# Performance work log

Hardware: AMD Instinct MI355X
Metric: run time of the kernel (lower is better)

## Reference

```python
import jax, jax.numpy as jnp
import numpy as np

BETA = 0.8
THRESHOLD = 1.0

@jax.custom_vjp
def surrogate_spike(m):
    return (m >= THRESHOLD).astype(m.dtype)

def _spike_fwd(m):
    return surrogate_spike(m), m

def _spike_bwd(m, g):
    s = jax.nn.sigmoid(4.0 * (m - THRESHOLD))
    return (g * s * (1.0 - s) * 4.0,)

surrogate_spike.defvjp(_spike_fwd, _spike_bwd)

def setup_inputs() -> dict:
    key = jax.random.key(0)
    k1, k2, k3, k4 = jax.random.split(key, 4)
    B, T, D, F = 4, 2048, 1024, 4096
    x = jax.random.normal(k1, (B, T, D), dtype=jnp.float32)
    Wg = jax.random.normal(k2, (F, D), dtype=jnp.float32) * (1.0 / np.sqrt(D))
    Wu = jax.random.normal(k3, (F, D), dtype=jnp.float32) * (1.0 / np.sqrt(D))
    Wd = jax.random.normal(k4, (D, F), dtype=jnp.float32) * (1.0 / np.sqrt(F))
    theta = jnp.ones((F,), dtype=jnp.float32) * THRESHOLD
    return {"x": x, "Wg": Wg, "Wu": Wu, "Wd": Wd, "theta": theta}

def reference(x, Wg, Wu, Wd, theta):
    # x: [B,T,D]; Wg,Wu: [F,D]; Wd: [D,F]; theta: [F]
    gate_input = jnp.einsum('btd,fd->btf', x, Wg)  # [B,T,F]

    def step(membrane, g_t):
        membrane = BETA * membrane + g_t           # leaky integrate
        spike = surrogate_spike(membrane)          # threshold fire
        membrane = membrane - theta * spike        # reset
        return membrane, spike

    B, T, F = gate_input.shape
    V0 = jnp.zeros((B, F), dtype=x.dtype)
    _, spikes = jax.lax.scan(step, V0, jnp.swapaxes(gate_input, 0, 1))  # [T,B,F]
    gate = jnp.swapaxes(spikes, 0, 1)              # [B,T,F]

    up = jnp.einsum('btd,fd->btf', x, Wu)
    return jnp.einsum('btf,df->btd', gate * jax.nn.silu(up), Wd)
```

## Files before the change

kernel.cpp:

```cpp
#include <hip/hip_runtime.h>
#include <hip/hip_bf16.h>
#include <math.h>


namespace {

constexpr int B_ = 4;
constexpr int T_ = 2048;
constexpr int D_ = 1024;
constexpr int F_ = 4096;
constexpr int TC = 512;
constexpr int NCHUNK = T_ / TC;
constexpr int MC = B_ * TC;
constexpr int LDK = 40;

typedef __attribute__((ext_vector_type(8))) short bf16x8;
typedef __attribute__((ext_vector_type(4))) float f32x4;
typedef __attribute__((ext_vector_type(2))) float f32x2;

#define PK_FMA_LO(accv, av, bv)                                         \
  asm("v_pk_fma_f32 %0, %1, %2, %0 op_sel:[0,0,0] op_sel_hi:[1,0,1]"    \
      : "+v"(accv) : "v"(av), "v"(bv))
#define PK_FMA_HI(accv, av, bv)                                         \
  asm("v_pk_fma_f32 %0, %1, %2, %0 op_sel:[0,1,0] op_sel_hi:[1,1,1]"    \
      : "+v"(accv) : "v"(av), "v"(bv))

__device__ __forceinline__ float silu_f(float u) {
  return u / (1.0f + expf(-u));
}

__device__ __forceinline__ int map_row(int r, int t0) {
  return (r >> 9) * T_ + t0 + (r & (TC - 1));
}

__device__ __forceinline__ unsigned short bf16_rn(float x) {
  unsigned int u = __float_as_uint(x);
  u += 0x7FFF + ((u >> 16) & 1);
  return (unsigned short)(u >> 16);
}
__device__ __forceinline__ float bf16_f(unsigned short h) {
  unsigned int u = ((unsigned int)h) << 16;
  return __uint_as_float(u);
}

__device__ __forceinline__ void async_copy16(const float* g, float* l) {
  __builtin_amdgcn_global_load_lds(
      (const __attribute__((address_space(1))) void*)g,
      (__attribute__((address_space(3))) void*)l, 16, 0, 0);
}

__global__ __launch_bounds__(256)
void transpose_wg(const float* __restrict__ Wg, float* __restrict__ WgT) {
  __shared__ float tile[32][33];
  const int tx = threadIdx.x & 31, ty = threadIdx.x >> 5;
  const int d0 = blockIdx.x * 32, f0 = blockIdx.y * 32;
#pragma unroll
  for (int i = 0; i < 4; ++i)
    tile[ty + i * 8][tx] = Wg[(size_t)(f0 + ty + i * 8) * D_ + d0 + tx];
  __syncthreads();
#pragma unroll
  for (int i = 0; i < 4; ++i)
    WgT[(size_t)(d0 + ty + i * 8) * F_ + f0 + tx] = tile[tx][ty + i * 8];
}

__global__ __launch_bounds__(256)
void transpose_x(const float* __restrict__ x, float* __restrict__ xT, int t0) {
  __shared__ float tile[32][33];
  const int tx = threadIdx.x & 31, ty = threadIdx.x >> 5;
  const int d0 = blockIdx.x * 32, r0 = blockIdx.y * 32;
#pragma unroll
  for (int i = 0; i < 4; ++i)
    tile[ty + i * 8][tx] =
        x[(size_t)map_row(r0 + ty + i * 8, t0) * D_ + d0 + tx];
  __syncthreads();
#pragma unroll
  for (int i = 0; i < 4; ++i)
    xT[(size_t)(d0 + ty + i * 8) * MC + r0 + tx] = tile[tx][ty + i * 8];
}

#pragma clang fp contract(off)
__global__ __launch_bounds__(512)
void gemm_gate_np(const float* __restrict__ xT, const float* __restrict__ WgT,
                  float* __restrict__ G) {
  __shared__ float As[32 * 128];
  __shared__ float Bs[32 * 128];
  const int tid = threadIdx.x;
  const int lane = tid & 63;
  const int w = tid >> 6;
  const int tx = tid & 31;
  const int ty = tid >> 5;
  const int row0 = blockIdx.y * 128;
  const int col0 = blockIdx.x * 128;

  f32x2 accP[4][4];
  f32x2 csumP[4][4];
#pragma unroll
  for (int i = 0; i < 4; ++i)
#pragma unroll
    for (int j = 0; j < 4; ++j) {
      accP[i][j] = (f32x2)0.0f;
      csumP[i][j] = (f32x2)0.0f;
    }

  for (int kt = 0; kt < D_; kt += 32) {
    if (kt != 0 && (kt & 127) == 0) {
#pragma unroll
      for (int i = 0; i < 4; ++i)
#pragma unroll
        for (int j = 0; j < 4; ++j) {
          csumP[i][j].x = __fadd_rn(csumP[i][j].x, accP[i][j].x);
          csumP[i][j].y = __fadd_rn(csumP[i][j].y, accP[i][j].y);
          accP[i][j] = (f32x2)0.0f;
        }
    }
    __syncthreads();
#pragma unroll
    for (int t = 0; t < 2; ++t) {
      const int ii = w * 2 + t;
      const int kr = kt + ii * 2 + (lane >> 5);
      async_copy16(&xT[(size_t)kr * MC + row0 + (lane & 31) * 4],
                   &As[ii * 256]);
    }
#pragma unroll
    for (int t = 0; t < 2; ++t) {
      const int ii = w * 2 + t;
      const int kr = kt + ii * 2 + (lane >> 5);
      async_copy16(&WgT[(size_t)kr * F_ + col0 + (lane & 31) * 4],
                   &Bs[ii * 256]);
    }
    __syncthreads();
#pragma unroll
    for (int kk = 0; kk < 32; ++kk) {
      const float4 a0 = *reinterpret_cast<const float4*>(&As[kk * 128 + ty * 8]);
      const float4 a1 = *reinterpret_cast<const float4*>(&As[kk * 128 + ty * 8 + 4]);
      const float4 b0 = *reinterpret_cast<const float4*>(&Bs[kk * 128 + tx * 4]);
      f32x2 ap[4];
      ap[0] = (f32x2){a0.x, a0.y};
      ap[1] = (f32x2){a0.z, a0.w};
      ap[2] = (f32x2){a1.x, a1.y};
      ap[3] = (f32x2){a1.z, a1.w};
      const f32x2 bp0 = (f32x2){b0.x, b0.y};
      const f32x2 bp1 = (f32x2){b0.z, b0.w};
#pragma unroll
      for (int ip = 0; ip < 4; ++ip) {
        PK_FMA_LO(accP[ip][0], ap[ip], bp0);
        PK_FMA_HI(accP[ip][1], ap[ip], bp0);
        PK_FMA_LO(accP[ip][2], ap[ip], bp1);
        PK_FMA_HI(accP[ip][3], ap[ip], bp1);
      }
    }
  }

#pragma unroll
  for (int ip = 0; ip < 4; ++ip) {
#pragma unroll
    for (int h = 0; h < 2; ++h) {
      const int r = row0 + ty * 8 + ip * 2 + h;
      float4 v;
      v.x = __fadd_rn(h ? csumP[ip][0].y : csumP[ip][0].x,
                      h ? accP[ip][0].y : accP[ip][0].x);
      v.y = __fadd_rn(h ? csumP[ip][1].y : csumP[ip][1].x,
                      h ? accP[ip][1].y : accP[ip][1].x);
      v.z = __fadd_rn(h ? csumP[ip][2].y : csumP[ip][2].x,
                      h ? accP[ip][2].y : accP[ip][2].x);
      v.w = __fadd_rn(h ? csumP[ip][3].y : csumP[ip][3].x,
                      h ? accP[ip][3].y : accP[ip][3].x);
      *reinterpret_cast<float4*>(&G[(size_t)r * F_ + col0 + tx * 4]) = v;
    }
  }
}
#pragma clang fp contract(fast)

#pragma clang fp contract(off)
__global__ __launch_bounds__(64)
void lif_scan(const float* __restrict__ G, unsigned char* __restrict__ S8,
              float* __restrict__ state, const float* __restrict__ theta,
              int t0) {
  const int j = blockIdx.x * 64 + threadIdx.x;
  const int f = j & (F_ - 1);
  const int b = j >> 12;
  float m = (t0 == 0) ? 0.0f : state[j];
  const float th = theta[f];
  const size_t base = (size_t)b * TC * F_ + f;
  for (int tb = 0; tb < TC; tb += 16) {
    float g[16];
#pragma unroll
    for (int u = 0; u < 16; ++u) g[u] = G[base + (size_t)(tb + u) * F_];
#pragma unroll
    for (int u = 0; u < 16; ++u) {
      const float bm = __fmul_rn(0.8f, m);
      m = __fadd_rn(bm, g[u]);
      const float s = (m >= 1.0f) ? 1.0f : 0.0f;
      const float r = __fmul_rn(th, s);
      m = __fsub_rn(m, r);
      S8[base + (size_t)(tb + u) * F_] = (unsigned char)s;
    }
  }
  state[j] = m;
}
#pragma clang fp contract(fast)

__global__ __launch_bounds__(256)
void cast_hi(const float* __restrict__ src, unsigned short* __restrict__ hi,
             int n4) {
  int i = blockIdx.x * 256 + threadIdx.x;
  const int stride = gridDim.x * 256;
  for (; i < n4; i += stride) {
    const float4 v = reinterpret_cast<const float4*>(src)[i];
    ushort4 h;
    h.x = bf16_rn(v.x);
    h.y = bf16_rn(v.y);
    h.z = bf16_rn(v.z);
    h.w = bf16_rn(v.w);
    reinterpret_cast<ushort4*>(hi)[i] = h;
  }
}

__global__ __launch_bounds__(256)
void split_x(const float* __restrict__ x, unsigned short* __restrict__ Xh,
             unsigned short* __restrict__ Xl, int t0) {
  const int i = blockIdx.x * 256 + threadIdx.x;
  const int r = i >> 8;
  const int q = i & 255;
  const float4 v = *reinterpret_cast<const float4*>(
      &x[(size_t)map_row(r, t0) * D_ + q * 4]);
  ushort4 h, l;
  h.x = bf16_rn(v.x); l.x = bf16_rn(v.x - bf16_f(h.x));
  h.y = bf16_rn(v.y); l.y = bf16_rn(v.y - bf16_f(h.y));
  h.z = bf16_rn(v.z); l.z = bf16_rn(v.z - bf16_f(h.z));
  h.w = bf16_rn(v.w); l.w = bf16_rn(v.w - bf16_f(h.w));
  *reinterpret_cast<ushort4*>(&Xh[(size_t)r * D_ + q * 4]) = h;
  *reinterpret_cast<ushort4*>(&Xl[(size_t)r * D_ + q * 4]) = l;
}

__global__ __launch_bounds__(256)
void up_mfma(const unsigned short* __restrict__ Xh,
             const unsigned short* __restrict__ Xl,
             const unsigned short* __restrict__ Wh,
             const unsigned char* __restrict__ S8,
             unsigned short* __restrict__ Hh, unsigned short* __restrict__ Hl) {
  __shared__ unsigned short Ah[128 * LDK], Al[128 * LDK];
  __shared__ unsigned short Bh[128 * LDK];
  const int tid = threadIdx.x;
  const int lane = tid & 63;
  const int w = tid >> 6;
  const int wr = (w >> 1) * 64;
  const int wc = (w & 1) * 64;
  const int brow = blockIdx.y * 128;
  const int bcol = blockIdx.x * 128;

  f32x4 acc[4][4];
#pragma unroll
  for (int i = 0; i < 4; ++i)
#pragma unroll
    for (int j = 0; j < 4; ++j) acc[i][j] = (f32x4)0.0f;

  for (int k0 = 0; k0 < D_; k0 += 32) {
    __syncthreads();
#pragma unroll
    for (int s = 0; s < 2; ++s) {
      const int v = tid + s * 256;
      const int row = v >> 2, q = v & 3;
      *reinterpret_cast<uint4*>(&Ah[row * LDK + q * 8]) =
          *reinterpret_cast<const uint4*>(
              &Xh[(size_t)(brow + row) * D_ + k0 + q * 8]);
      *reinterpret_cast<uint4*>(&Al[row * LDK + q * 8]) =
          *reinterpret_cast<const uint4*>(
              &Xl[(size_t)(brow + row) * D_ + k0 + q * 8]);
      *reinterpret_cast<uint4*>(&Bh[row * LDK + q * 8]) =
          *reinterpret_cast<const uint4*>(
              &Wh[(size_t)(bcol + row) * D_ + k0 + q * 8]);
    }
    __syncthreads();
    const int fr = lane & 15;
    const int kq = (lane >> 4) * 8;
    bf16x8 ah[4], al[4], bh[4];
#pragma unroll
    for (int i = 0; i < 4; ++i) {
      ah[i] = *reinterpret_cast<const bf16x8*>(&Ah[(wr + i * 16 + fr) * LDK + kq]);
      al[i] = *reinterpret_cast<const bf16x8*>(&Al[(wr + i * 16 + fr) * LDK + kq]);
      bh[i] = *reinterpret_cast<const bf16x8*>(&Bh[(wc + i * 16 + fr) * LDK + kq]);
    }
#pragma unroll
    for (int i = 0; i < 4; ++i)
#pragma unroll
      for (int j = 0; j < 4; ++j) {
        acc[i][j] = __builtin_amdgcn_mfma_f32_16x16x32_bf16(ah[i], bh[j], acc[i][j], 0, 0, 0);
        acc[i][j] = __builtin_amdgcn_mfma_f32_16x16x32_bf16(al[i], bh[j], acc[i][j], 0, 0, 0);
      }
  }

  const int fr = lane & 15;
  const int rg = (lane >> 4) * 4;
#pragma unroll
  for (int i = 0; i < 4; ++i)
#pragma unroll
    for (int j = 0; j < 4; ++j) {
      const int c = bcol + wc + j * 16 + fr;
#pragma unroll
      for (int r = 0; r < 4; ++r) {
        const int rl = brow + wr + i * 16 + rg + r;
        const float up = acc[i][j][r];
        const float h = S8[(size_t)rl * F_ + c] ? silu_f(up) : 0.0f;
        const unsigned short hh = bf16_rn(h);
        Hh[(size_t)rl * F_ + c] = hh;
        Hl[(size_t)rl * F_ + c] = bf16_rn(h - bf16_f(hh));
      }
    }
}

__global__ __launch_bounds__(256)
void down_mfma(const unsigned short* __restrict__ Hh,
               const unsigned short* __restrict__ Hl,
               const unsigned short* __restrict__ Wh,
               float* __restrict__ out, int t0) {
  __shared__ unsigned short Ah[128 * LDK], Al[128 * LDK];
  __shared__ unsigned short Bh[64 * LDK];
  const int tid = threadIdx.x;
  const int lane = tid & 63;
  const int w = tid >> 6;
  const int wr = (w >> 1) * 64;
  const int wc = (w & 1) * 32;
  const int brow = blockIdx.y * 128;
  const int bcol = blockIdx.x * 64;

  f32x4 acc[4][2];
#pragma unroll
  for (int i = 0; i < 4; ++i)
#pragma unroll
    for (int j = 0; j < 2; ++j) acc[i][j] = (f32x4)0.0f;

  for (int k0 = 0; k0 < F_; k0 += 32) {
    __syncthreads();
#pragma unroll
    for (int s = 0; s < 2; ++s) {
      const int v = tid + s * 256;
      const int row = v >> 2, q = v & 3;
      *reinterpret_cast<uint4*>(&Ah[row * LDK + q * 8]) =
          *reinterpret_cast<const uint4*>(
              &Hh[(size_t)(brow + row) * F_ + k0 + q * 8]);
      *reinterpret_cast<uint4*>(&Al[row * LDK + q * 8]) =
          *reinterpret_cast<const uint4*>(
              &Hl[(size_t)(brow + row) * F_ + k0 + q * 8]);
    }
    {
      const int row = tid >> 2, q = tid & 3;
      *reinterpret_cast<uint4*>(&Bh[row * LDK + q * 8]) =
          *reinterpret_cast<const uint4*>(
              &Wh[(size_t)(bcol + row) * F_ + k0 + q * 8]);
    }
    __syncthreads();
    const int fr = lane & 15;
    const int kq = (lane >> 4) * 8;
    bf16x8 ah[4], al[4], bh[2];
#pragma unroll
    for (int i = 0; i < 4; ++i) {
      ah[i] = *reinterpret_cast<const bf16x8*>(&Ah[(wr + i * 16 + fr) * LDK + kq]);
      al[i] = *reinterpret_cast<const bf16x8*>(&Al[(wr + i * 16 + fr) * LDK + kq]);
    }
#pragma unroll
    for (int j = 0; j < 2; ++j)
      bh[j] = *reinterpret_cast<const bf16x8*>(&Bh[(wc + j * 16 + fr) * LDK + kq]);
#pragma unroll
    for (int i = 0; i < 4; ++i)
#pragma unroll
      for (int j = 0; j < 2; ++j) {
        acc[i][j] = __builtin_amdgcn_mfma_f32_16x16x32_bf16(ah[i], bh[j], acc[i][j], 0, 0, 0);
        acc[i][j] = __builtin_amdgcn_mfma_f32_16x16x32_bf16(al[i], bh[j], acc[i][j], 0, 0, 0);
      }
  }

  const int fr = lane & 15;
  const int rg = (lane >> 4) * 4;
#pragma unroll
  for (int i = 0; i < 4; ++i)
#pragma unroll
    for (int j = 0; j < 2; ++j) {
      const int c = bcol + wc + j * 16 + fr;
#pragma unroll
      for (int r = 0; r < 4; ++r) {
        const int rl = brow + wr + i * 16 + rg + r;
        out[(size_t)map_row(rl, t0) * D_ + c] = acc[i][j][r];
      }
    }
}

}

extern "C" void kernel_launch(void* const* d_in, const int* in_sizes, int n_in,
                              void* d_out, int out_size, void* d_ws,
                              size_t ws_size, hipStream_t stream) {
  const float* x = (const float*)d_in[0];
  const float* Wg = (const float*)d_in[1];
  const float* Wu = (const float*)d_in[2];
  const float* Wd = (const float*)d_in[3];
  const float* theta = (const float*)d_in[4];
  float* out = (float*)d_out;

  char* ws = (char*)d_ws;
  const size_t wu_b = (size_t)F_ * D_ * 2;
  unsigned short* Wu_hi = (unsigned short*)ws;
  unsigned short* Wd_hi = (unsigned short*)(ws + wu_b);
  float* WgT = (float*)(ws + 2 * wu_b);
  char* xbase = ws + 2 * wu_b + (size_t)F_ * D_ * 4;
  unsigned short* Xh = (unsigned short*)xbase;
  unsigned short* Xl = (unsigned short*)(xbase + (size_t)MC * D_ * 2);
  char* gbase = xbase + (size_t)MC * D_ * 4;
  float* G = (float*)gbase;
  unsigned short* Hh = (unsigned short*)gbase;
  unsigned short* Hl = (unsigned short*)(gbase + (size_t)MC * F_ * 2);
  char* s8xt = gbase + (size_t)MC * F_ * 4;
  float* xT = (float*)s8xt;
  unsigned char* S8 = (unsigned char*)s8xt;
  float* state = (float*)(s8xt + (size_t)MC * D_ * 4);

  const dim3 blk(256);
  hipLaunchKernelGGL(cast_hi, dim3(1024), blk, 0, stream, Wu, Wu_hi,
                     F_ * D_ / 4);
  hipLaunchKernelGGL(cast_hi, dim3(1024), blk, 0, stream, Wd, Wd_hi,
                     D_ * F_ / 4);
  hipLaunchKernelGGL(transpose_wg, dim3(D_ / 32, F_ / 32), blk, 0, stream,
                     Wg, WgT);

  const dim3 g_tx(D_ / 32, MC / 32);
  const dim3 g_gt(F_ / 128, MC / 128);
  const dim3 g_sc(B_ * F_ / 64);
  const dim3 g_sx(MC * D_ / 4 / 256);
  const dim3 g_up(F_ / 128, MC / 128);
  const dim3 g_dn(D_ / 64, MC / 128);

  for (int c = 0; c < NCHUNK; ++c) {
    const int t0 = c * TC;
    hipLaunchKernelGGL(transpose_x, g_tx, blk, 0, stream, x, xT, t0);
    hipLaunchKernelGGL(split_x, g_sx, blk, 0, stream, x, Xh, Xl, t0);
    hipLaunchKernelGGL(gemm_gate_np, g_gt, dim3(512), 0, stream, xT, WgT, G);
    hipLaunchKernelGGL(lif_scan, g_sc, dim3(64), 0, stream, G, S8, state,
                       theta, t0);
    hipLaunchKernelGGL(up_mfma, g_up, blk, 0, stream, Xh, Xl, Wu_hi,
                       S8, Hh, Hl);
    hipLaunchKernelGGL(down_mfma, g_dn, blk, 0, stream, Hh, Hl, Wd_hi,
                       out, t0);
  }
}
```

Baseline: 1.528 ms.

## Double-buffer gate GEMM LDS tiles and fuse x transpose with bf16 split

The fp32 gate GEMM now keeps two LDS buffers per operand. It issues the async global-to-LDS copy for the next k-slice before computing on the current one, using a single barrier per iteration, so memory latency can overlap the packed FMA work. Separately, the x transpose and the hi/lo bf16 split are merged into one prep_x kernel that reads each x chunk once with float4 loads and writes both xT and Xh/Xl. This saves one kernel launch and one pass over x per chunk. The cost is double the LDS per GEMM block, which may reduce occupancy.

```diff
diff --git a/kernel.cpp b/kernel.cpp
--- a/kernel.cpp
+++ b/kernel.cpp
@@ -64,26 +64,42 @@
 }
 
 __global__ __launch_bounds__(256)
-void transpose_x(const float* __restrict__ x, float* __restrict__ xT, int t0) {
+void prep_x(const float* __restrict__ x, float* __restrict__ xT,
+            unsigned short* __restrict__ Xh, unsigned short* __restrict__ Xl,
+            int t0) {
   __shared__ float tile[32][33];
-  const int tx = threadIdx.x & 31, ty = threadIdx.x >> 5;
+  const int tx = threadIdx.x & 7;
+  const int ty = threadIdx.x >> 3;
   const int d0 = blockIdx.x * 32, r0 = blockIdx.y * 32;
-#pragma unroll
-  for (int i = 0; i < 4; ++i)
-    tile[ty + i * 8][tx] =
-        x[(size_t)map_row(r0 + ty + i * 8, t0) * D_ + d0 + tx];
+
+  const float4 v = *reinterpret_cast<const float4*>(
+      &x[(size_t)map_row(r0 + ty, t0) * D_ + d0 + tx * 4]);
+  ushort4 h, l;
+  h.x = bf16_rn(v.x); l.x = bf16_rn(v.x - bf16_f(h.x));
+  h.y = bf16_rn(v.y); l.y = bf16_rn(v.y - bf16_f(h.y));
+  h.z = bf16_rn(v.z); l.z = bf16_rn(v.z - bf16_f(h.z));
+  h.w = bf16_rn(v.w); l.w = bf16_rn(v.w - bf16_f(h.w));
+  *reinterpret_cast<ushort4*>(&Xh[(size_t)(r0 + ty) * D_ + d0 + tx * 4]) = h;
+  *reinterpret_cast<ushort4*>(&Xl[(size_t)(r0 + ty) * D_ + d0 + tx * 4]) = l;
+  tile[ty][tx * 4 + 0] = v.x;
+  tile[ty][tx * 4 + 1] = v.y;
+  tile[ty][tx * 4 + 2] = v.z;
+  tile[ty][tx * 4 + 3] = v.w;
   __syncthreads();
-#pragma unroll
-  for (int i = 0; i < 4; ++i)
-    xT[(size_t)(d0 + ty + i * 8) * MC + r0 + tx] = tile[tx][ty + i * 8];
+  float4 w;
+  w.x = tile[tx * 4 + 0][ty];
+  w.y = tile[tx * 4 + 1][ty];
+  w.z = tile[tx * 4 + 2][ty];
+  w.w = tile[tx * 4 + 3][ty];
+  *reinterpret_cast<float4*>(&xT[(size_t)(d0 + ty) * MC + r0 + tx * 4]) = w;
 }
 
 #pragma clang fp contract(off)
 __global__ __launch_bounds__(512)
 void gemm_gate_np(const float* __restrict__ xT, const float* __restrict__ WgT,
                   float* __restrict__ G) {
-  __shared__ float As[32 * 128];
-  __shared__ float Bs[32 * 128];
+  __shared__ float As[2][32 * 128];
+  __shared__ float Bs[2][32 * 128];
   const int tid = threadIdx.x;
   const int lane = tid & 63;
   const int w = tid >> 6;
@@ -102,8 +118,32 @@
       csumP[i][j] = (f32x2)0.0f;
     }
 
-  for (int kt = 0; kt < D_; kt += 32) {
-    if (kt != 0 && (kt & 127) == 0) {
+  const int a_off = (tid >> 6) * 2;
+  const int lr = (lane & 31) * 4;
+  const int lh = lane >> 5;
+
+  auto stage = [&](int kt32, int buf) {
+    const int kt = kt32 * 32;
+#pragma unroll
+    for (int t = 0; t < 2; ++t) {
+      const int ii = a_off + t;
+      const int kr = kt + ii * 2 + lh;
+      async_copy16(&xT[(size_t)kr * MC + row0 + lr], &As[buf][ii * 256]);
+    }
+#pragma unroll
+    for (int t = 0; t < 2; ++t) {
+      const int ii = a_off + t;
+      const int kr = kt + ii * 2 + lh;
+      async_copy16(&WgT[(size_t)kr * F_ + col0 + lr], &Bs[buf][ii * 256]);
+    }
+  };
+
+  stage(0, 0);
+  __syncthreads();
+  int cur = 0;
+
+  for (int kt32 = 0; kt32 < 32; ++kt32) {
+    if (kt32 != 0 && (kt32 & 3) == 0) {
 #pragma unroll
       for (int i = 0; i < 4; ++i)
 #pragma unroll
@@ -113,27 +153,12 @@
           accP[i][j] = (f32x2)0.0f;
         }
     }
-    __syncthreads();
-#pragma unroll
-    for (int t = 0; t < 2; ++t) {
-      const int ii = w * 2 + t;
-      const int kr = kt + ii * 2 + (lane >> 5);
-      async_copy16(&xT[(size_t)kr * MC + row0 + (lane & 31) * 4],
-                   &As[ii * 256]);
-    }
-#pragma unroll
-    for (int t = 0; t < 2; ++t) {
-      const int ii = w * 2 + t;
-      const int kr = kt + ii * 2 + (lane >> 5);
-      async_copy16(&WgT[(size_t)kr * F_ + col0 + (lane & 31) * 4],
-                   &Bs[ii * 256]);
-    }
-    __syncthreads();
+    if (kt32 + 1 < 32) stage(kt32 + 1, cur ^ 1);
 #pragma unroll
     for (int kk = 0; kk < 32; ++kk) {
-      const float4 a0 = *reinterpret_cast<const float4*>(&As[kk * 128 + ty * 8]);
-      const float4 a1 = *reinterpret_cast<const float4*>(&As[kk * 128 + ty * 8 + 4]);
-      const float4 b0 = *reinterpret_cast<const float4*>(&Bs[kk * 128 + tx * 4]);
+      const float4 a0 = *reinterpret_cast<const float4*>(&As[cur][kk * 128 + ty * 8]);
+      const float4 a1 = *reinterpret_cast<const float4*>(&As[cur][kk * 128 + ty * 8 + 4]);
+      const float4 b0 = *reinterpret_cast<const float4*>(&Bs[cur][kk * 128 + tx * 4]);
       f32x2 ap[4];
       ap[0] = (f32x2){a0.x, a0.y};
       ap[1] = (f32x2){a0.z, a0.w};
@@ -149,6 +174,8 @@
         PK_FMA_HI(accP[ip][3], ap[ip], bp1);
       }
     }
+    __syncthreads();
+    cur ^= 1;
   }
 
 #pragma unroll
@@ -214,23 +241,6 @@
     h.w = bf16_rn(v.w);
     reinterpret_cast<ushort4*>(hi)[i] = h;
   }
-}
-
-__global__ __launch_bounds__(256)
-void split_x(const float* __restrict__ x, unsigned short* __restrict__ Xh,
-             unsigned short* __restrict__ Xl, int t0) {
-  const int i = blockIdx.x * 256 + threadIdx.x;
-  const int r = i >> 8;
-  const int q = i & 255;
-  const float4 v = *reinterpret_cast<const float4*>(
-      &x[(size_t)map_row(r, t0) * D_ + q * 4]);
-  ushort4 h, l;
-  h.x = bf16_rn(v.x); l.x = bf16_rn(v.x - bf16_f(h.x));
-  h.y = bf16_rn(v.y); l.y = bf16_rn(v.y - bf16_f(h.y));
-  h.z = bf16_rn(v.z); l.z = bf16_rn(v.z - bf16_f(h.z));
-  h.w = bf16_rn(v.w); l.w = bf16_rn(v.w - bf16_f(h.w));
-  *reinterpret_cast<ushort4*>(&Xh[(size_t)r * D_ + q * 4]) = h;
-  *reinterpret_cast<ushort4*>(&Xl[(size_t)r * D_ + q * 4]) = l;
 }
 
 __global__ __launch_bounds__(256)
@@ -422,17 +432,15 @@
   hipLaunchKernelGGL(transpose_wg, dim3(D_ / 32, F_ / 32), blk, 0, stream,
                      Wg, WgT);
 
-  const dim3 g_tx(D_ / 32, MC / 32);
+  const dim3 g_px(D_ / 32, MC / 32);
   const dim3 g_gt(F_ / 128, MC / 128);
   const dim3 g_sc(B_ * F_ / 64);
-  const dim3 g_sx(MC * D_ / 4 / 256);
   const dim3 g_up(F_ / 128, MC / 128);
   const dim3 g_dn(D_ / 64, MC / 128);
 
   for (int c = 0; c < NCHUNK; ++c) {
     const int t0 = c * TC;
-    hipLaunchKernelGGL(transpose_x, g_tx, blk, 0, stream, x, xT, t0);
-    hipLaunchKernelGGL(split_x, g_sx, blk, 0, stream, x, Xh, Xl, t0);
+    hipLaunchKernelGGL(prep_x, g_px, blk, 0, stream, x, xT, Xh, Xl, t0);
     hipLaunchKernelGGL(gemm_gate_np, g_gt, dim3(512), 0, stream, xT, WgT, G);
     hipLaunchKernelGGL(lif_scan, g_sc, dim3(64), 0, stream, G, S8, state,
                        theta, t0);
```

Result: no change. 1.509 ms (-1.2%).
